# Optimization experiments

Hardware: AMD Instinct MI355X
Metric: run time of the kernel (lower is better)

## Reference

```python
import jax, jax.numpy as jnp
import numpy as np

N = 50000       # nodes
E = 800000      # edges (no self-loops; conv adds them)
IN = 128        # in_channels
HID = 128       # hidden_channels
HEADS = 4
OUT = 64        # out_channels (classes)
THR = 0.1       # cosine-similarity threshold
COS_EPS = 1e-8  # torch F.cosine_similarity eps
LN_EPS = 1e-5


def _glorot(key, shape):
    lim = np.sqrt(6.0 / (shape[0] + shape[1]))
    return jax.random.uniform(key, shape, jnp.float32, -lim, lim)


def setup_inputs() -> dict:
    key = jax.random.key(0)
    ks = jax.random.split(key, 8)
    x = jax.random.normal(ks[0], (N, IN), jnp.float32)
    # edges with src != dst (module removes self-loops then re-adds all N)
    src = jax.random.randint(ks[1], (E,), 0, N)
    off = jax.random.randint(ks[2], (E,), 1, N)
    dst = (src + off) % N
    edge_index = jnp.stack([src, dst]).astype(jnp.int64)
    return {
        "x": x,
        "edge_index": edge_index,
        "W0": _glorot(ks[3], (IN, HID)),  "b0": jnp.zeros((HID,), jnp.float32),
        "W1": _glorot(ks[4], (HID, HID)), "b1": jnp.zeros((HID,), jnp.float32),
        "W2": _glorot(ks[5], (HID, OUT)), "b2": jnp.zeros((OUT,), jnp.float32),
        "g1": jnp.ones((HID,), jnp.float32), "be1": jnp.zeros((HID,), jnp.float32),
        "g2": jnp.ones((HID,), jnp.float32), "be2": jnp.zeros((HID,), jnp.float32),
    }


def _cosine(a, b):
    dot = jnp.sum(a * b, axis=-1)
    na = jnp.maximum(jnp.linalg.norm(a, axis=-1), COS_EPS)
    nb = jnp.maximum(jnp.linalg.norm(b, axis=-1), COS_EPS)
    return dot / (na * nb)


def _layernorm(x, g, b):
    m = jnp.mean(x, axis=-1, keepdims=True)
    v = jnp.mean(jnp.square(x - m), axis=-1, keepdims=True)
    return (x - m) * jax.lax.rsqrt(v + LN_EPS) * g + b


def _rgat_conv(x, src, dst, W, bias, heads, thr):
    n = x.shape[0]
    hc = W.shape[1]
    c = hc // heads
    # add self loops (input edges contain none)
    loop = jnp.arange(n, dtype=src.dtype)
    s = jnp.concatenate([src, loop])
    d = jnp.concatenate([dst, loop])
    xl = (x @ W).reshape(n, heads, c)                      # [N,H,C]
    # cosine-similarity attention on raw features, thresholded
    a = _cosine(x[d], x[s])                                # [Etot]
    a = jnp.where(a < thr, 1e-6, a)
    # segment softmax of log(a) over destination == a / segment_sum(a)
    denom = jax.ops.segment_sum(a, d, num_segments=n)      # [N]
    alpha = a / denom[d]                                   # [Etot]
    msg = xl[s] * alpha[:, None, None]                     # [Etot,H,C]
    out = jax.ops.segment_sum(msg, d, num_segments=n)      # [N,H,C]
    return out.reshape(n, hc) + bias                       # concat heads


def reference(x, edge_index, W0, b0, W1, b1, W2, b2, g1, be1, g2, be2):
    src, dst = edge_index[0], edge_index[1]
    h = _rgat_conv(x, src, dst, W0, b0, HEADS, THR)
    h = jax.nn.relu(_layernorm(h, g1, be1))
    h = _rgat_conv(h, src, dst, W1, b1, HEADS, THR)
    h = jax.nn.relu(_layernorm(h, g2, be2))
    h = _rgat_conv(h, src, dst, W2, b2, 1, THR)
    return jax.nn.log_softmax(h, axis=-1)
```

## Files before the change

kernel.cpp:

```cpp
#include <hip/hip_runtime.h>
#include <hip/hip_bf16.h>

#define THR 0.1f
#define COS_EPS 1e-8f
#define LN_EPS 1e-5f

__device__ __forceinline__ float wave_sum(float v) {
    #pragma unroll
    for (int o = 1; o < 64; o <<= 1) v += __shfl_xor(v, o);
    return v;
}
__device__ __forceinline__ float gsum16(float v) {
    #pragma unroll
    for (int o = 1; o < 16; o <<= 1) v += __shfl_xor(v, o);
    return v;
}
__device__ __forceinline__ float gsum8(float v) {
    #pragma unroll
    for (int o = 1; o < 8; o <<= 1) v += __shfl_xor(v, o);
    return v;
}
__device__ __forceinline__ float gmax8(float v) {
    #pragma unroll
    for (int o = 1; o < 8; o <<= 1) v = fmaxf(v, __shfl_xor(v, o));
    return v;
}

__global__ void count_k(const int* __restrict__ dst, int E, int* __restrict__ counts) {
    int e = blockIdx.x * 256 + threadIdx.x;
    if (e < E) atomicAdd(&counts[dst[e]], 1);
}

__global__ void scan1_k(const int* __restrict__ counts, int* __restrict__ partials, int ntot) {
    int base = blockIdx.x * 1024;
    int t = threadIdx.x;
    int s = 0;
    #pragma unroll
    for (int i = 0; i < 4; ++i) {
        int idx = base + t + i * 256;
        if (idx < ntot) s += counts[idx];
    }
    s = (int)wave_sum((float)s);
    __shared__ int ws[4];
    if ((t & 63) == 0) ws[t >> 6] = s;
    __syncthreads();
    if (t == 0) partials[blockIdx.x] = ws[0] + ws[1] + ws[2] + ws[3];
}

__global__ void scan2_k(int* __restrict__ partials, int nb) {
    int t = threadIdx.x;
    int v = (t < nb) ? partials[t] : 0;
    int orig = v;
    #pragma unroll
    for (int o = 1; o < 64; o <<= 1) {
        int u = __shfl_up(v, o);
        if (t >= o) v += u;
    }
    if (t < nb) partials[t] = v - orig;
}

__global__ void scan3_k(int* __restrict__ counts, const int* __restrict__ partials,
                        int* __restrict__ offs, int ntot) {
    int base = blockIdx.x * 1024;
    int t = threadIdx.x;
    int lane = t & 63, wid = t >> 6;
    int idx = base + t * 4;
    int c[4];
    #pragma unroll
    for (int k = 0; k < 4; ++k) c[k] = (idx + k < ntot) ? counts[idx + k] : 0;
    int s = c[0] + c[1] + c[2] + c[3];
    int sc = s;
    #pragma unroll
    for (int o = 1; o < 64; o <<= 1) {
        int u = __shfl_up(sc, o);
        if (lane >= o) sc += u;
    }
    __shared__ int wsum[4];
    if (lane == 63) wsum[wid] = sc;
    __syncthreads();
    int add = partials[blockIdx.x];
    for (int w = 0; w < wid; ++w) add += wsum[w];
    int ex = add + sc - s;
    #pragma unroll
    for (int k = 0; k < 4; ++k) {
        if (idx + k < ntot) {
            offs[idx + k] = ex;
            counts[idx + k] = ex;
            ex += c[k];
        }
    }
}

__global__ void scatter_k(const int* __restrict__ src, const int* __restrict__ dst, int E,
                          int* __restrict__ cursor, int* __restrict__ csr_src) {
    int e = blockIdx.x * 256 + threadIdx.x;
    if (e < E) {
        int p = atomicAdd(&cursor[dst[e]], 1);
        csr_src[p] = src[e];
    }
}

__global__ void normpack_k(const float* __restrict__ h, float* __restrict__ hn,
                           float* __restrict__ norms, int n) {
    int node = (blockIdx.x * blockDim.x + threadIdx.x) >> 6;
    int lane = threadIdx.x & 63;
    if (node >= n) return;
    float2 v = *(const float2*)(h + (size_t)node * 128 + lane * 2);
    float ss = wave_sum(v.x * v.x + v.y * v.y);
    float nrm = sqrtf(ss);
    float inv = 1.0f / fmaxf(nrm, COS_EPS);
    float2 o = {v.x * inv, v.y * inv};
    *(float2*)(hn + (size_t)node * 128 + lane * 2) = o;
    if (lane == 0) norms[node] = nrm;
}

__global__ void agg_k(const float* __restrict__ hn, const float* __restrict__ norms,
                      const int* __restrict__ offs, const int* __restrict__ csr,
                      float* __restrict__ r, int n) {
    int node = (blockIdx.x * blockDim.x + threadIdx.x) >> 6;
    int lane = threadIdx.x & 63;
    if (node >= n) return;
    int g = lane >> 4;
    int q = lane & 15;
    const float* myrow = hn + (size_t)node * 128 + q * 8;
    float4 d0 = *(const float4*)myrow;
    float4 d1 = *(const float4*)(myrow + 4);
    float nd = norms[node];
    float p = d0.x * d0.x + d0.y * d0.y + d0.z * d0.z + d0.w * d0.w
            + d1.x * d1.x + d1.y * d1.y + d1.z * d1.z + d1.w * d1.w;
    p = gsum16(p);
    float4 a0 = {0.f, 0.f, 0.f, 0.f}, a1 = {0.f, 0.f, 0.f, 0.f};
    float denom = 0.f;
    int b = offs[node], e = offs[node + 1];
    for (int i0 = b; i0 < e; i0 += 64) {
        int cnt = e - i0;
        if (cnt > 64) cnt = 64;
        int sidx = csr[i0 + (lane < cnt ? lane : 0)];
        int jp = (g < cnt) ? g : 0;
        int s = __shfl(sidx, jp);
        const float* sp = hn + (size_t)s * 128 + q * 8;
        float4 h0 = *(const float4*)sp;
        float4 h1 = *(const float4*)(sp + 4);
        float ns = norms[s];
        for (int j = 0; j < cnt; j += 4) {
            float4 c0 = h0, c1 = h1;
            float cn = ns;
            int jn = j + 4 + g;
            jn = (jn < cnt) ? jn : 0;
            int s2 = __shfl(sidx, jn);
            const float* sp2 = hn + (size_t)s2 * 128 + q * 8;
            h0 = *(const float4*)sp2;
            h1 = *(const float4*)(sp2 + 4);
            ns = norms[s2];
            float t = d0.x * c0.x + d0.y * c0.y + d0.z * c0.z + d0.w * c0.w
                    + d1.x * c1.x + d1.y * c1.y + d1.z * c1.z + d1.w * c1.w;
            t = gsum16(t);
            if (j + g < cnt) {
                float av = (t < THR) ? 1e-6f : t;
                denom += av;
                float w = av * cn;
                a0.x += w * c0.x; a0.y += w * c0.y; a0.z += w * c0.z; a0.w += w * c0.w;
                a1.x += w * c1.x; a1.y += w * c1.y; a1.z += w * c1.z; a1.w += w * c1.w;
            }
        }
    }
    #pragma unroll
    for (int o = 16; o < 64; o <<= 1) {
        a0.x += __shfl_xor(a0.x, o); a0.y += __shfl_xor(a0.y, o);
        a0.z += __shfl_xor(a0.z, o); a0.w += __shfl_xor(a0.w, o);
        a1.x += __shfl_xor(a1.x, o); a1.y += __shfl_xor(a1.y, o);
        a1.z += __shfl_xor(a1.z, o); a1.w += __shfl_xor(a1.w, o);
        denom += __shfl_xor(denom, o);
    }
    float a = (p < THR) ? 1e-6f : p;
    denom += a;
    float w = a * nd;
    a0.x += w * d0.x; a0.y += w * d0.y; a0.z += w * d0.z; a0.w += w * d0.w;
    a1.x += w * d1.x; a1.y += w * d1.y; a1.z += w * d1.z; a1.w += w * d1.w;
    if (g == 0) {
        float inv = 1.0f / denom;
        float4 o0 = {a0.x * inv, a0.y * inv, a0.z * inv, a0.w * inv};
        float4 o1 = {a1.x * inv, a1.y * inv, a1.z * inv, a1.w * inv};
        *(float4*)(r + (size_t)node * 128 + q * 8) = o0;
        *(float4*)(r + (size_t)node * 128 + q * 8 + 4) = o1;
    }
}

__global__ void gemm_ln_k(const float* __restrict__ A, const float* __restrict__ B,
                          const float* __restrict__ bias, const float* __restrict__ g,
                          const float* __restrict__ be, float* __restrict__ hn,
                          float* __restrict__ norms, int M) {
    __shared__ float sA[64][33];
    __shared__ float sB[32][136];
    int row0 = blockIdx.x * 64;
    int tid = threadIdx.x;
    int tx = tid & 15, ty = tid >> 4;
    float acc[4][8];
    #pragma unroll
    for (int r = 0; r < 4; ++r)
        #pragma unroll
        for (int j = 0; j < 8; ++j) acc[r][j] = 0.f;

    for (int k0 = 0; k0 < 128; k0 += 32) {
        for (int i = tid; i < 64 * 32; i += 256) {
            int r = i >> 5, c = i & 31;
            sA[r][c] = (row0 + r < M) ? A[(size_t)(row0 + r) * 128 + k0 + c] : 0.f;
        }
        for (int i = tid; i < 32 * 128; i += 256) {
            int r = i >> 7, c = i & 127;
            sB[r][c] = B[(size_t)(k0 + r) * 128 + c];
        }
        __syncthreads();
        #pragma unroll
        for (int kk = 0; kk < 32; ++kk) {
            float4 bb0 = *(const float4*)&sB[kk][tx * 8];
            float4 bb1 = *(const float4*)&sB[kk][tx * 8 + 4];
            #pragma unroll
            for (int r = 0; r < 4; ++r) {
                float a = sA[ty * 4 + r][kk];
                acc[r][0] += a * bb0.x; acc[r][1] += a * bb0.y;
                acc[r][2] += a * bb0.z; acc[r][3] += a * bb0.w;
                acc[r][4] += a * bb1.x; acc[r][5] += a * bb1.y;
                acc[r][6] += a * bb1.z; acc[r][7] += a * bb1.w;
            }
        }
        __syncthreads();
    }
    float4 b4a = *(const float4*)(bias + tx * 8);
    float4 b4b = *(const float4*)(bias + tx * 8 + 4);
    float4 g4a = *(const float4*)(g + tx * 8);
    float4 g4b = *(const float4*)(g + tx * 8 + 4);
    float4 e4a = *(const float4*)(be + tx * 8);
    float4 e4b = *(const float4*)(be + tx * 8 + 4);
    #pragma unroll
    for (int r = 0; r < 4; ++r) {
        int row = row0 + ty * 4 + r;
        float o[8];
        float ls = 0.f;
        #pragma unroll
        for (int j = 0; j < 8; ++j) {
            o[j] = acc[r][j] + (j < 4 ? (&b4a.x)[j] : (&b4b.x)[j - 4]);
            ls += o[j];
        }
        float m = gsum16(ls) * (1.0f / 128.f);
        float vv = 0.f;
        float d[8];
        #pragma unroll
        for (int j = 0; j < 8; ++j) {
            d[j] = o[j] - m;
            vv += d[j] * d[j];
        }
        float var = gsum16(vv) * (1.0f / 128.f);
        float rs = rsqrtf(var + LN_EPS);
        float y[8];
        float ss = 0.f;
        #pragma unroll
        for (int j = 0; j < 8; ++j) {
            float gj = (j < 4 ? (&g4a.x)[j] : (&g4b.x)[j - 4]);
            float ej = (j < 4 ? (&e4a.x)[j] : (&e4b.x)[j - 4]);
            y[j] = fmaxf(d[j] * rs * gj + ej, 0.f);
            ss += y[j] * y[j];
        }
        float sst = gsum16(ss);
        float nrm = sqrtf(sst);
        float inv = 1.0f / fmaxf(nrm, COS_EPS);
        if (row < M) {
            float4 o0 = {y[0] * inv, y[1] * inv, y[2] * inv, y[3] * inv};
            float4 o1 = {y[4] * inv, y[5] * inv, y[6] * inv, y[7] * inv};
            *(float4*)(hn + (size_t)row * 128 + tx * 8) = o0;
            *(float4*)(hn + (size_t)row * 128 + tx * 8 + 4) = o1;
            if (tx == 0) norms[row] = nrm;
        }
    }
}

__global__ void gemm_lsm_k(const float* __restrict__ A, const float* __restrict__ B,
                           const float* __restrict__ bias, float* __restrict__ out, int M) {
    __shared__ float sA[64][33];
    __shared__ float sB[32][72];
    int row0 = blockIdx.x * 64;
    int tid = threadIdx.x;
    int tx = tid & 7, ty = tid >> 3;
    float acc[2][8];
    #pragma unroll
    for (int r = 0; r < 2; ++r)
        #pragma unroll
        for (int j = 0; j < 8; ++j) acc[r][j] = 0.f;

    for (int k0 = 0; k0 < 128; k0 += 32) {
        for (int i = tid; i < 64 * 32; i += 256) {
            int r = i >> 5, c = i & 31;
            sA[r][c] = (row0 + r < M) ? A[(size_t)(row0 + r) * 128 + k0 + c] : 0.f;
        }
        for (int i = tid; i < 32 * 64; i += 256) {
            int r = i >> 6, c = i & 63;
            sB[r][c] = B[(size_t)(k0 + r) * 64 + c];
        }
        __syncthreads();
        #pragma unroll
        for (int kk = 0; kk < 32; ++kk) {
            float4 bb0 = *(const float4*)&sB[kk][tx * 8];
            float4 bb1 = *(const float4*)&sB[kk][tx * 8 + 4];
            #pragma unroll
            for (int r = 0; r < 2; ++r) {
                float a = sA[ty * 2 + r][kk];
                acc[r][0] += a * bb0.x; acc[r][1] += a * bb0.y;
                acc[r][2] += a * bb0.z; acc[r][3] += a * bb0.w;
                acc[r][4] += a * bb1.x; acc[r][5] += a * bb1.y;
                acc[r][6] += a * bb1.z; acc[r][7] += a * bb1.w;
            }
        }
        __syncthreads();
    }
    float4 b4a = *(const float4*)(bias + tx * 8);
    float4 b4b = *(const float4*)(bias + tx * 8 + 4);
    #pragma unroll
    for (int r = 0; r < 2; ++r) {
        int row = row0 + ty * 2 + r;
        float v[8];
        float mx = -1e30f;
        #pragma unroll
        for (int j = 0; j < 8; ++j) {
            v[j] = acc[r][j] + (j < 4 ? (&b4a.x)[j] : (&b4b.x)[j - 4]);
            mx = fmaxf(mx, v[j]);
        }
        float m = gmax8(mx);
        float es = 0.f;
        #pragma unroll
        for (int j = 0; j < 8; ++j) es += __expf(v[j] - m);
        float s = gsum8(es);
        float ls = logf(s);
        if (row < M) {
            float4 o0 = {v[0] - m - ls, v[1] - m - ls, v[2] - m - ls, v[3] - m - ls};
            float4 o1 = {v[4] - m - ls, v[5] - m - ls, v[6] - m - ls, v[7] - m - ls};
            *(float4*)(out + (size_t)row * 64 + tx * 8) = o0;
            *(float4*)(out + (size_t)row * 64 + tx * 8 + 4) = o1;
        }
    }
}

extern "C" void kernel_launch(void* const* d_in, const int* in_sizes, int n_in,
                              void* d_out, int out_size, void* d_ws, size_t ws_size,
                              hipStream_t stream) {
    const float* x  = (const float*)d_in[0];
    const int* ei   = (const int*)d_in[1];
    const float* W0 = (const float*)d_in[2];
    const float* b0 = (const float*)d_in[3];
    const float* W1 = (const float*)d_in[4];
    const float* b1 = (const float*)d_in[5];
    const float* W2 = (const float*)d_in[6];
    const float* b2 = (const float*)d_in[7];
    const float* g1 = (const float*)d_in[8];
    const float* be1 = (const float*)d_in[9];
    const float* g2 = (const float*)d_in[10];
    const float* be2 = (const float*)d_in[11];

    const int N = in_sizes[0] / 128;
    const int E = in_sizes[1] / 2;
    const int* src = ei;
    const int* dst = ei + E;
    const int ntot = N + 1;
    const int nscan = (ntot + 1023) / 1024;

    size_t off = 0;
    auto carve = [&](size_t bytes) {
        void* p = (char*)d_ws + off;
        off += (bytes + 255) & ~(size_t)255;
        return p;
    };
    float* bufA   = (float*)carve((size_t)N * 128 * 4);
    float* bufB   = (float*)carve((size_t)N * 128 * 4);
    float* nA     = (float*)carve((size_t)N * 4);
    float* nB     = (float*)carve((size_t)N * 4);
    int* counts   = (int*)carve((size_t)ntot * 4);
    int* offs     = (int*)carve((size_t)ntot * 4);
    int* partials = (int*)carve((size_t)256 * 4);
    int* csr      = (int*)carve((size_t)E * 4);

    hipMemsetAsync(counts, 0, (size_t)ntot * 4, stream);
    count_k<<<(E + 255) / 256, 256, 0, stream>>>(dst, E, counts);
    scan1_k<<<nscan, 256, 0, stream>>>(counts, partials, ntot);
    scan2_k<<<1, 64, 0, stream>>>(partials, nscan);
    scan3_k<<<nscan, 256, 0, stream>>>(counts, partials, offs, ntot);
    scatter_k<<<(E + 255) / 256, 256, 0, stream>>>(src, dst, E, counts, csr);

    const int gridN4 = (N + 3) / 4;
    const int gridG = (N + 63) / 64;

    normpack_k<<<gridN4, 256, 0, stream>>>(x, bufA, nA, N);
    agg_k<<<gridN4, 256, 0, stream>>>(bufA, nA, offs, csr, bufB, N);
    gemm_ln_k<<<gridG, 256, 0, stream>>>(bufB, W0, b0, g1, be1, bufB, nB, N);

    agg_k<<<gridN4, 256, 0, stream>>>(bufB, nB, offs, csr, bufA, N);
    gemm_ln_k<<<gridG, 256, 0, stream>>>(bufA, W1, b1, g2, be2, bufA, nA, N);

    agg_k<<<gridN4, 256, 0, stream>>>(bufA, nA, offs, csr, bufB, N);
    gemm_lsm_k<<<gridG, 256, 0, stream>>>(bufB, W2, b2, (float*)d_out, N);
}
```

Measured before the change: 418.0 us.

## Replace FP32 SIMT GEMMs with split-bf16 MFMA GEMMs; deepen agg prefetch

Each dense layer GEMM now runs on bf16 MFMA instructions. Both operands are split into three bf16 parts (hi/mid/lo) and six cross products are summed, which emulates FP32 accuracy. Weights are pre-split into fragment-ordered planes by a small prep kernel, and each wave computes a 16-row tile straight from global memory without shared memory. The aggregation kernel also prefetches neighbor rows two iterations ahead instead of one, to hide gather latency. The cost is more register pressure and six times the MFMA work, and the output stores become narrower scalar writes.

```diff
diff --git a/kernel.cpp b/kernel.cpp
--- a/kernel.cpp
+++ b/kernel.cpp
@@ -5,6 +5,9 @@
 #define COS_EPS 1e-8f
 #define LN_EPS 1e-5f
 
+typedef short bfx8 __attribute__((ext_vector_type(8)));
+typedef float fx4 __attribute__((ext_vector_type(4)));
+
 __device__ __forceinline__ float wave_sum(float v) {
     #pragma unroll
     for (int o = 1; o < 64; o <<= 1) v += __shfl_xor(v, o);
@@ -15,15 +18,19 @@
     for (int o = 1; o < 16; o <<= 1) v += __shfl_xor(v, o);
     return v;
 }
-__device__ __forceinline__ float gsum8(float v) {
-    #pragma unroll
-    for (int o = 1; o < 8; o <<= 1) v += __shfl_xor(v, o);
+__device__ __forceinline__ float gmax16(float v) {
+    #pragma unroll
+    for (int o = 1; o < 16; o <<= 1) v = fmaxf(v, __shfl_xor(v, o));
     return v;
 }
-__device__ __forceinline__ float gmax8(float v) {
-    #pragma unroll
-    for (int o = 1; o < 8; o <<= 1) v = fmaxf(v, __shfl_xor(v, o));
-    return v;
+
+__device__ __forceinline__ unsigned short f2bf(float f) {
+    unsigned int u = __float_as_uint(f);
+    unsigned int r = (u + 0x7FFFu + ((u >> 16) & 1u)) >> 16;
+    return (unsigned short)r;
+}
+__device__ __forceinline__ float bf2f(unsigned short h) {
+    return __uint_as_float(((unsigned int)h) << 16);
 }
 
 __global__ void count_k(const int* __restrict__ dst, int E, int* __restrict__ counts) {
@@ -136,22 +143,28 @@
         int cnt = e - i0;
         if (cnt > 64) cnt = 64;
         int sidx = csr[i0 + (lane < cnt ? lane : 0)];
-        int jp = (g < cnt) ? g : 0;
-        int s = __shfl(sidx, jp);
-        const float* sp = hn + (size_t)s * 128 + q * 8;
-        float4 h0 = *(const float4*)sp;
-        float4 h1 = *(const float4*)(sp + 4);
-        float ns = norms[s];
+        int jp0 = (g < cnt) ? g : 0;
+        int s0 = __shfl(sidx, jp0);
+        const float* sp0 = hn + (size_t)s0 * 128 + q * 8;
+        float4 e0a = *(const float4*)sp0, e0b = *(const float4*)(sp0 + 4);
+        float e0n = norms[s0];
+        int jp1 = 4 + g;
+        jp1 = (jp1 < cnt) ? jp1 : 0;
+        int s1 = __shfl(sidx, jp1);
+        const float* sp1 = hn + (size_t)s1 * 128 + q * 8;
+        float4 e1a = *(const float4*)sp1, e1b = *(const float4*)(sp1 + 4);
+        float e1n = norms[s1];
         for (int j = 0; j < cnt; j += 4) {
-            float4 c0 = h0, c1 = h1;
-            float cn = ns;
-            int jn = j + 4 + g;
+            float4 c0 = e0a, c1 = e0b;
+            float cn = e0n;
+            e0a = e1a; e0b = e1b; e0n = e1n;
+            int jn = j + 8 + g;
             jn = (jn < cnt) ? jn : 0;
             int s2 = __shfl(sidx, jn);
             const float* sp2 = hn + (size_t)s2 * 128 + q * 8;
-            h0 = *(const float4*)sp2;
-            h1 = *(const float4*)(sp2 + 4);
-            ns = norms[s2];
+            e1a = *(const float4*)sp2;
+            e1b = *(const float4*)(sp2 + 4);
+            e1n = norms[s2];
             float t = d0.x * c0.x + d0.y * c0.y + d0.z * c0.z + d0.w * c0.w
                     + d1.x * c1.x + d1.y * c1.y + d1.z * c1.z + d1.w * c1.w;
             t = gsum16(t);
@@ -186,155 +199,176 @@
     }
 }
 
-__global__ void gemm_ln_k(const float* __restrict__ A, const float* __restrict__ B,
-                          const float* __restrict__ bias, const float* __restrict__ g,
-                          const float* __restrict__ be, float* __restrict__ hn,
-                          float* __restrict__ norms, int M) {
-    __shared__ float sA[64][33];
-    __shared__ float sB[32][136];
-    int row0 = blockIdx.x * 64;
-    int tid = threadIdx.x;
-    int tx = tid & 15, ty = tid >> 4;
-    float acc[4][8];
-    #pragma unroll
-    for (int r = 0; r < 4; ++r)
-        #pragma unroll
-        for (int j = 0; j < 8; ++j) acc[r][j] = 0.f;
-
-    for (int k0 = 0; k0 < 128; k0 += 32) {
-        for (int i = tid; i < 64 * 32; i += 256) {
-            int r = i >> 5, c = i & 31;
-            sA[r][c] = (row0 + r < M) ? A[(size_t)(row0 + r) * 128 + k0 + c] : 0.f;
-        }
-        for (int i = tid; i < 32 * 128; i += 256) {
-            int r = i >> 7, c = i & 127;
-            sB[r][c] = B[(size_t)(k0 + r) * 128 + c];
-        }
-        __syncthreads();
-        #pragma unroll
-        for (int kk = 0; kk < 32; ++kk) {
-            float4 bb0 = *(const float4*)&sB[kk][tx * 8];
-            float4 bb1 = *(const float4*)&sB[kk][tx * 8 + 4];
-            #pragma unroll
-            for (int r = 0; r < 4; ++r) {
-                float a = sA[ty * 4 + r][kk];
-                acc[r][0] += a * bb0.x; acc[r][1] += a * bb0.y;
-                acc[r][2] += a * bb0.z; acc[r][3] += a * bb0.w;
-                acc[r][4] += a * bb1.x; acc[r][5] += a * bb1.y;
-                acc[r][6] += a * bb1.z; acc[r][7] += a * bb1.w;
+template <int CF>
+__global__ __launch_bounds__(256) void wprep_k(const float* __restrict__ W,
+                                               unsigned short* __restrict__ P) {
+    const int PLANE = CF * 2048;
+    int t = blockIdx.x * 256 + threadIdx.x;
+    if (t >= 4 * CF * 64) return;
+    int lane = t & 63, fr = t >> 6;
+    int cf = fr % CF, ks = fr / CF;
+    int col = cf * 16 + (lane & 15);
+    int k0 = ks * 32 + (lane >> 4) * 8;
+    size_t base = (size_t)fr * 512 + (size_t)lane * 8;
+    #pragma unroll
+    for (int j = 0; j < 8; ++j) {
+        float x = W[(size_t)(k0 + j) * (CF * 16) + col];
+        unsigned short h = f2bf(x);
+        float fh = bf2f(h);
+        float r1 = x - fh;
+        unsigned short m = f2bf(r1);
+        float fm = bf2f(m);
+        unsigned short lo = f2bf(r1 - fm);
+        P[base + j] = h;
+        P[PLANE + base + j] = m;
+        P[2 * PLANE + base + j] = lo;
+    }
+}
+
+template <int CF>
+__device__ __forceinline__ void mfma_core(const float* __restrict__ arow,
+                                          const unsigned short* __restrict__ P,
+                                          int lane, fx4* acc) {
+    const int PLANE = CF * 2048;
+    float ast[32];
+    #pragma unroll
+    for (int ks = 0; ks < 4; ++ks) {
+        float4 u0 = *(const float4*)(arow + ks * 32);
+        float4 u1 = *(const float4*)(arow + ks * 32 + 4);
+        ast[ks * 8 + 0] = u0.x; ast[ks * 8 + 1] = u0.y;
+        ast[ks * 8 + 2] = u0.z; ast[ks * 8 + 3] = u0.w;
+        ast[ks * 8 + 4] = u1.x; ast[ks * 8 + 5] = u1.y;
+        ast[ks * 8 + 6] = u1.z; ast[ks * 8 + 7] = u1.w;
+    }
+    #pragma unroll
+    for (int ks = 0; ks < 4; ++ks) {
+        bfx8 ah, am, al;
+        #pragma unroll
+        for (int j = 0; j < 8; ++j) {
+            float x = ast[ks * 8 + j];
+            unsigned short h = f2bf(x);
+            float fh = bf2f(h);
+            float r1 = x - fh;
+            unsigned short m = f2bf(r1);
+            float fm = bf2f(m);
+            unsigned short lo = f2bf(r1 - fm);
+            ah[j] = (short)h; am[j] = (short)m; al[j] = (short)lo;
+        }
+        #pragma unroll
+        for (int cb = 0; cb < CF; cb += 4) {
+            bfx8 bh[4], bm[4], bl[4];
+            #pragma unroll
+            for (int q = 0; q < 4; ++q) {
+                size_t base = ((size_t)(ks * CF + cb + q) * 64 + lane) * 8;
+                bh[q] = *(const bfx8*)(P + base);
+                bm[q] = *(const bfx8*)(P + PLANE + base);
+                bl[q] = *(const bfx8*)(P + 2 * PLANE + base);
             }
-        }
-        __syncthreads();
-    }
-    float4 b4a = *(const float4*)(bias + tx * 8);
-    float4 b4b = *(const float4*)(bias + tx * 8 + 4);
-    float4 g4a = *(const float4*)(g + tx * 8);
-    float4 g4b = *(const float4*)(g + tx * 8 + 4);
-    float4 e4a = *(const float4*)(be + tx * 8);
-    float4 e4b = *(const float4*)(be + tx * 8 + 4);
+            #pragma unroll
+            for (int q = 0; q < 4; ++q)
+                acc[cb + q] = __builtin_amdgcn_mfma_f32_16x16x32_bf16(ah, bh[q], acc[cb + q], 0, 0, 0);
+            #pragma unroll
+            for (int q = 0; q < 4; ++q)
+                acc[cb + q] = __builtin_amdgcn_mfma_f32_16x16x32_bf16(ah, bm[q], acc[cb + q], 0, 0, 0);
+            #pragma unroll
+            for (int q = 0; q < 4; ++q)
+                acc[cb + q] = __builtin_amdgcn_mfma_f32_16x16x32_bf16(am, bh[q], acc[cb + q], 0, 0, 0);
+            #pragma unroll
+            for (int q = 0; q < 4; ++q)
+                acc[cb + q] = __builtin_amdgcn_mfma_f32_16x16x32_bf16(ah, bl[q], acc[cb + q], 0, 0, 0);
+            #pragma unroll
+            for (int q = 0; q < 4; ++q)
+                acc[cb + q] = __builtin_amdgcn_mfma_f32_16x16x32_bf16(am, bm[q], acc[cb + q], 0, 0, 0);
+            #pragma unroll
+            for (int q = 0; q < 4; ++q)
+                acc[cb + q] = __builtin_amdgcn_mfma_f32_16x16x32_bf16(al, bh[q], acc[cb + q], 0, 0, 0);
+        }
+    }
+}
+
+__global__ __launch_bounds__(256) void mgemm_ln_k(const float* __restrict__ A,
+    const unsigned short* __restrict__ P, const float* __restrict__ bias,
+    const float* __restrict__ g, const float* __restrict__ be,
+    float* __restrict__ hn, float* __restrict__ norms, int nw, int M) {
+    const int CF = 8;
+    int wid = blockIdx.x * 4 + (threadIdx.x >> 6);
+    if (wid >= nw) return;
+    int lane = threadIdx.x & 63;
+    int rsel = lane & 15, kg = lane >> 4;
+    int arowi = wid * 16 + rsel;
+    if (arowi >= M) arowi = M - 1;
+    const float* arow = A + (size_t)arowi * 128 + kg * 8;
+    fx4 acc[CF];
+    #pragma unroll
+    for (int c = 0; c < CF; ++c) acc[c] = (fx4){0.f, 0.f, 0.f, 0.f};
+    mfma_core<CF>(arow, P, lane, acc);
+    float bi[CF], gm[CF], bb[CF];
+    #pragma unroll
+    for (int c = 0; c < CF; ++c) {
+        int col = c * 16 + rsel;
+        bi[c] = bias[col]; gm[c] = g[col]; bb[c] = be[col];
+    }
     #pragma unroll
     for (int r = 0; r < 4; ++r) {
-        int row = row0 + ty * 4 + r;
-        float o[8];
-        float ls = 0.f;
-        #pragma unroll
-        for (int j = 0; j < 8; ++j) {
-            o[j] = acc[r][j] + (j < 4 ? (&b4a.x)[j] : (&b4b.x)[j - 4]);
-            ls += o[j];
-        }
-        float m = gsum16(ls) * (1.0f / 128.f);
+        int row = wid * 16 + kg * 4 + r;
+        float o[CF], s = 0.f;
+        #pragma unroll
+        for (int c = 0; c < CF; ++c) { o[c] = acc[c][r] + bi[c]; s += o[c]; }
+        float mean = gsum16(s) * (1.f / 128.f);
         float vv = 0.f;
-        float d[8];
-        #pragma unroll
-        for (int j = 0; j < 8; ++j) {
-            d[j] = o[j] - m;
-            vv += d[j] * d[j];
-        }
-        float var = gsum16(vv) * (1.0f / 128.f);
+        #pragma unroll
+        for (int c = 0; c < CF; ++c) { o[c] -= mean; vv += o[c] * o[c]; }
+        float var = gsum16(vv) * (1.f / 128.f);
         float rs = rsqrtf(var + LN_EPS);
-        float y[8];
         float ss = 0.f;
         #pragma unroll
-        for (int j = 0; j < 8; ++j) {
-            float gj = (j < 4 ? (&g4a.x)[j] : (&g4b.x)[j - 4]);
-            float ej = (j < 4 ? (&e4a.x)[j] : (&e4b.x)[j - 4]);
-            y[j] = fmaxf(d[j] * rs * gj + ej, 0.f);
-            ss += y[j] * y[j];
-        }
-        float sst = gsum16(ss);
-        float nrm = sqrtf(sst);
-        float inv = 1.0f / fmaxf(nrm, COS_EPS);
+        for (int c = 0; c < CF; ++c) {
+            o[c] = fmaxf(o[c] * rs * gm[c] + bb[c], 0.f);
+            ss += o[c] * o[c];
+        }
+        float nrm = sqrtf(gsum16(ss));
+        float inv = 1.f / fmaxf(nrm, COS_EPS);
         if (row < M) {
-            float4 o0 = {y[0] * inv, y[1] * inv, y[2] * inv, y[3] * inv};
-            float4 o1 = {y[4] * inv, y[5] * inv, y[6] * inv, y[7] * inv};
-            *(float4*)(hn + (size_t)row * 128 + tx * 8) = o0;
-            *(float4*)(hn + (size_t)row * 128 + tx * 8 + 4) = o1;
-            if (tx == 0) norms[row] = nrm;
-        }
-    }
-}
-
-__global__ void gemm_lsm_k(const float* __restrict__ A, const float* __restrict__ B,
-                           const float* __restrict__ bias, float* __restrict__ out, int M) {
-    __shared__ float sA[64][33];
-    __shared__ float sB[32][72];
-    int row0 = blockIdx.x * 64;
-    int tid = threadIdx.x;
-    int tx = tid & 7, ty = tid >> 3;
-    float acc[2][8];
-    #pragma unroll
-    for (int r = 0; r < 2; ++r)
-        #pragma unroll
-        for (int j = 0; j < 8; ++j) acc[r][j] = 0.f;
-
-    for (int k0 = 0; k0 < 128; k0 += 32) {
-        for (int i = tid; i < 64 * 32; i += 256) {
-            int r = i >> 5, c = i & 31;
-            sA[r][c] = (row0 + r < M) ? A[(size_t)(row0 + r) * 128 + k0 + c] : 0.f;
-        }
-        for (int i = tid; i < 32 * 64; i += 256) {
-            int r = i >> 6, c = i & 63;
-            sB[r][c] = B[(size_t)(k0 + r) * 64 + c];
-        }
-        __syncthreads();
-        #pragma unroll
-        for (int kk = 0; kk < 32; ++kk) {
-            float4 bb0 = *(const float4*)&sB[kk][tx * 8];
-            float4 bb1 = *(const float4*)&sB[kk][tx * 8 + 4];
-            #pragma unroll
-            for (int r = 0; r < 2; ++r) {
-                float a = sA[ty * 2 + r][kk];
-                acc[r][0] += a * bb0.x; acc[r][1] += a * bb0.y;
-                acc[r][2] += a * bb0.z; acc[r][3] += a * bb0.w;
-                acc[r][4] += a * bb1.x; acc[r][5] += a * bb1.y;
-                acc[r][6] += a * bb1.z; acc[r][7] += a * bb1.w;
-            }
-        }
-        __syncthreads();
-    }
-    float4 b4a = *(const float4*)(bias + tx * 8);
-    float4 b4b = *(const float4*)(bias + tx * 8 + 4);
-    #pragma unroll
-    for (int r = 0; r < 2; ++r) {
-        int row = row0 + ty * 2 + r;
-        float v[8];
-        float mx = -1e30f;
-        #pragma unroll
-        for (int j = 0; j < 8; ++j) {
-            v[j] = acc[r][j] + (j < 4 ? (&b4a.x)[j] : (&b4b.x)[j - 4]);
-            mx = fmaxf(mx, v[j]);
-        }
-        float m = gmax8(mx);
+            #pragma unroll
+            for (int c = 0; c < CF; ++c) hn[(size_t)row * 128 + c * 16 + rsel] = o[c] * inv;
+            if (rsel == 0) norms[row] = nrm;
+        }
+    }
+}
+
+__global__ __launch_bounds__(256) void mgemm_lsm_k(const float* __restrict__ A,
+    const unsigned short* __restrict__ P, const float* __restrict__ bias,
+    float* __restrict__ out, int nw, int M) {
+    const int CF = 4;
+    int wid = blockIdx.x * 4 + (threadIdx.x >> 6);
+    if (wid >= nw) return;
+    int lane = threadIdx.x & 63;
+    int rsel = lane & 15, kg = lane >> 4;
+    int arowi = wid * 16 + rsel;
+    if (arowi >= M) arowi = M - 1;
+    const float* arow = A + (size_t)arowi * 128 + kg * 8;
+    fx4 acc[CF];
+    #pragma unroll
+    for (int c = 0; c < CF; ++c) acc[c] = (fx4){0.f, 0.f, 0.f, 0.f};
+    mfma_core<CF>(arow, P, lane, acc);
+    float bi[CF];
+    #pragma unroll
+    for (int c = 0; c < CF; ++c) bi[c] = bias[c * 16 + rsel];
+    #pragma unroll
+    for (int r = 0; r < 4; ++r) {
+        int row = wid * 16 + kg * 4 + r;
+        float v[CF], mx = -1e30f;
+        #pragma unroll
+        for (int c = 0; c < CF; ++c) { v[c] = acc[c][r] + bi[c]; mx = fmaxf(mx, v[c]); }
+        float m = gmax16(mx);
         float es = 0.f;
         #pragma unroll
-        for (int j = 0; j < 8; ++j) es += __expf(v[j] - m);
-        float s = gsum8(es);
+        for (int c = 0; c < CF; ++c) es += __expf(v[c] - m);
+        float s = gsum16(es);
         float ls = logf(s);
         if (row < M) {
-            float4 o0 = {v[0] - m - ls, v[1] - m - ls, v[2] - m - ls, v[3] - m - ls};
-            float4 o1 = {v[4] - m - ls, v[5] - m - ls, v[6] - m - ls, v[7] - m - ls};
-            *(float4*)(out + (size_t)row * 64 + tx * 8) = o0;
-            *(float4*)(out + (size_t)row * 64 + tx * 8 + 4) = o1;
+            #pragma unroll
+            for (int c = 0; c < CF; ++c) out[(size_t)row * 64 + c * 16 + rsel] = v[c] - m - ls;
         }
     }
 }
@@ -376,6 +410,13 @@
     int* offs     = (int*)carve((size_t)ntot * 4);
     int* partials = (int*)carve((size_t)256 * 4);
     int* csr      = (int*)carve((size_t)E * 4);
+    unsigned short* w0p = (unsigned short*)carve((size_t)3 * 16384 * 2);
+    unsigned short* w1p = (unsigned short*)carve((size_t)3 * 16384 * 2);
+    unsigned short* w2p = (unsigned short*)carve((size_t)3 * 8192 * 2);
+
+    wprep_k<8><<<8, 256, 0, stream>>>(W0, w0p);
+    wprep_k<8><<<8, 256, 0, stream>>>(W1, w1p);
+    wprep_k<4><<<4, 256, 0, stream>>>(W2, w2p);
 
     hipMemsetAsync(counts, 0, (size_t)ntot * 4, stream);
     count_k<<<(E + 255) / 256, 256, 0, stream>>>(dst, E, counts);
@@ -385,15 +426,16 @@
     scatter_k<<<(E + 255) / 256, 256, 0, stream>>>(src, dst, E, counts, csr);
 
     const int gridN4 = (N + 3) / 4;
-    const int gridG = (N + 63) / 64;
+    const int nwaves = (N + 15) / 16;
+    const int gridW = (nwaves + 3) / 4;
 
     normpack_k<<<gridN4, 256, 0, stream>>>(x, bufA, nA, N);
     agg_k<<<gridN4, 256, 0, stream>>>(bufA, nA, offs, csr, bufB, N);
-    gemm_ln_k<<<gridG, 256, 0, stream>>>(bufB, W0, b0, g1, be1, bufB, nB, N);
+    mgemm_ln_k<<<gridW, 256, 0, stream>>>(bufB, w0p, b0, g1, be1, bufB, nB, nwaves, N);
 
     agg_k<<<gridN4, 256, 0, stream>>>(bufB, nB, offs, csr, bufA, N);
-    gemm_ln_k<<<gridG, 256, 0, stream>>>(bufA, W1, b1, g2, be2, bufA, nA, N);
+    mgemm_ln_k<<<gridW, 256, 0, stream>>>(bufA, w1p, b1, g2, be2, bufA, nA, nwaves, N);
 
     agg_k<<<gridN4, 256, 0, stream>>>(bufA, nA, offs, csr, bufB, N);
-    gemm_lsm_k<<<gridG, 256, 0, stream>>>(bufB, W2, b2, (float*)d_out, N);
-}
+    mgemm_lsm_k<<<gridW, 256, 0, stream>>>(bufB, w2p, b2, (float*)d_out, nwaves, N);
+}
```

Measured after the change: 360.6 us. 1.16x faster.
